# Performance work log

Hardware: AMD Instinct MI355X
Metric: run time of the kernel (lower is better)

## Reference

```python
import jax, jax.numpy as jnp
import numpy as np

N, M, D = 100000, 5000, 2

def setup_inputs() -> dict:
    key = jax.random.key(0)
    k1, k2, k3 = jax.random.split(key, 3)
    euclidean_data = jax.random.normal(k1, (N, D), dtype=jnp.float32)
    maze_points = jax.random.normal(k2, (M, D), dtype=jnp.float32)
    ts_proj = jax.random.uniform(k3, (M,), dtype=jnp.float32)
    return {"euclidean_data": euclidean_data, "maze_points": maze_points, "ts_proj": ts_proj}

def reference(euclidean_data, maze_points, ts_proj):
    # squared distance matrix [N, M], reduced via argmin (1-NN)
    diff = euclidean_data[:, None, :] - maze_points[None, :, :]   # [N, M, D]
    dist2 = jnp.sum(jnp.square(diff), axis=-1)                    # [N, M]
    best = jnp.argmin(dist2, axis=1)                              # [N]
    projected_pos = maze_points[best]                             # [N, D]
    linear_pos = ts_proj[best]                                    # [N]
    return (projected_pos, linear_pos)
```

## Files before the change

### kernel.cpp

```cpp
#include <hip/hip_runtime.h>

#define N_Q  100000
#define N_M  5000
#define CW   4
#define CHK  1264
#define NSUB 79
#define NPAD (CW * CHK)
#define WS_BYTES (NPAD * 2 * 4)

typedef float v2f __attribute__((ext_vector_type(2)));
typedef float v8f __attribute__((ext_vector_type(8)));

__global__ void setup_soa(const float* __restrict__ maze, float* __restrict__ ws) {
    const int i = blockIdx.x * 256 + threadIdx.x;
    if (i >= NPAD) return;
    const int c = i / CHK, k = i - c * CHK;
    float x = 1e30f, y = 1e30f;
    const int g = c * 1250 + k;
    if (k < 1250) { x = -maze[2 * g]; y = -maze[2 * g + 1]; }
    ws[i] = x;
    ws[NPAD + i] = y;
}

#define LDX0(D) asm volatile("s_load_dwordx8 %0, %1, 0x0"    : "=s"(D) : "s"(xb))
#define LDX1(D) asm volatile("s_load_dwordx8 %0, %1, 0x20"   : "=s"(D) : "s"(xb))
#define LDY0(D) asm volatile("s_load_dwordx8 %0, %1, 0x4f00" : "=s"(D) : "s"(xb))
#define LDY1(D) asm volatile("s_load_dwordx8 %0, %1, 0x4f20" : "=s"(D) : "s"(xb))
#define WAIT4(a,b,c,d) asm volatile("s_waitcnt lgkmcnt(0)" : "+s"(a), "+s"(b), "+s"(c), "+s"(d))

#define PSTEP(X8, Y8, J) do {                                                 \
    v2f px_ = __builtin_shufflevector(X8, X8, 2*(J), 2*(J)+1);                \
    v2f py_ = __builtin_shufflevector(Y8, Y8, 2*(J), 2*(J)+1);                \
    v2f dx_, dy_;                                                             \
    asm("v_pk_add_f32 %0, %1, %2" : "=v"(dx_) : "s"(px_), "v"(qxx));          \
    asm("v_pk_add_f32 %0, %1, %2" : "=v"(dy_) : "s"(py_), "v"(qyy));          \
    asm("v_pk_mul_f32 %0, %0, %0" : "+v"(dx_));                               \
    asm("v_pk_mul_f32 %0, %0, %0" : "+v"(dy_));                               \
    asm("v_pk_add_f32 %0, %0, %1" : "+v"(dx_) : "v"(dy_));                    \
    float a_ = dx_.x, b_ = dx_.y;                                             \
    asm("v_min3_f32 %0, %1, %2, %0" : "+v"(bm) : "v"(a_), "v"(b_));           \
} while (0)

#define COMP(X0, X1, Y0, Y1, B) do {                                          \
    PSTEP(X0, Y0, 0); PSTEP(X0, Y0, 1); PSTEP(X0, Y0, 2); PSTEP(X0, Y0, 3);   \
    PSTEP(X1, Y1, 0); PSTEP(X1, Y1, 1); PSTEP(X1, Y1, 2); PSTEP(X1, Y1, 3);   \
    bb = (bm < prev) ? (B) : bb; prev = bm;                                   \
} while (0)

__global__ __launch_bounds__(256) void nn_scan(
    const float* __restrict__ q,
    const float* __restrict__ maze,
    const float* __restrict__ ts,
    const float* __restrict__ ws,
    float* __restrict__ out)
{
    __shared__ float sval[CW][64];
    __shared__ int   sidx[CW][64];

    const int lane = threadIdx.x & 63;
    const int wv   = __builtin_amdgcn_readfirstlane((int)(threadIdx.x >> 6));
    const int qi   = blockIdx.x * 64 + lane;
    const int qc   = qi < N_Q ? qi : N_Q - 1;

    const float2 Q = ((const float2*)q)[qc];
    const v2f qxx = { Q.x, Q.x };
    const v2f qyy = { Q.y, Q.y };

    unsigned long long xb =
        (unsigned long long)(const void*)(ws + (size_t)wv * CHK);

    v8f ax0, ax1, ay0, ay1, bx0, bx1, by0, by1;
    LDX0(ax0); LDX1(ax1); LDY0(ay0); LDY1(ay1); xb += 64;

    float bm = 3.4e38f, prev = 3.4e38f;
    int bb = 0;

    #pragma unroll 1
    for (int k = 0; k < 39; ++k) {
        WAIT4(ax0, ax1, ay0, ay1);
        LDX0(bx0); LDX1(bx1); LDY0(by0); LDY1(by1); xb += 64;
        COMP(ax0, ax1, ay0, ay1, 2 * k);
        WAIT4(bx0, bx1, by0, by1);
        LDX0(ax0); LDX1(ax1); LDY0(ay0); LDY1(ay1); xb += 64;
        COMP(bx0, bx1, by0, by1, 2 * k + 1);
    }
    WAIT4(ax0, ax1, ay0, ay1);
    COMP(ax0, ax1, ay0, ay1, 78);

    int fk = 0x7fffffff;
    {
        const float* xs = ws + (size_t)wv * CHK + (size_t)bb * 16;
        #pragma unroll
        for (int j = 0; j < 16; ++j) {
            const float dx = __fadd_rn(Q.x, xs[j]);
            const float dy = __fadd_rn(Q.y, xs[j + NPAD]);
            const float d2 = __fadd_rn(__fmul_rn(dx, dx), __fmul_rn(dy, dy));
            if (d2 == bm) fk = min(fk, bb * 16 + j);
        }
    }
    const int kloc = fk < 1250 ? fk : 1249;
    sval[wv][lane] = bm;
    sidx[wv][lane] = wv * 1250 + kloc;
    __syncthreads();

    if (wv == 0 && qi < N_Q) {
        float bv = sval[0][lane];
        int   bg = sidx[0][lane];
        #pragma unroll
        for (int c = 1; c < CW; ++c) {
            const float v = sval[c][lane];
            const int   g = sidx[c][lane];
            if (v < bv || (v == bv && g < bg)) { bv = v; bg = g; }
        }
        const float2 bp = ((const float2*)maze)[bg];
        out[2 * qi]       = bp.x;
        out[2 * qi + 1]   = bp.y;
        out[2 * N_Q + qi] = ts[bg];
    }
}

#define FCH   8
#define FLCH  640
#define FNP   (FCH * FLCH)
#define FSUB  16
#define FNSUB (FLCH / FSUB)
#define FFPS  (FSUB / 2)

#define FPK_ADD(d, a, b) asm("v_pk_add_f32 %0, %1, %2" : "=v"(d) : "v"(a), "v"(b))
#define FPK_MUL(d, a, b) asm("v_pk_mul_f32 %0, %1, %2" : "=v"(d) : "v"(a), "v"(b))
#define FMIN3(d, a, b, c) asm("v_min3_f32 %0, %1, %2, %3" : "=v"(d) : "v"(a), "v"(b), "v"(c))

__global__ __launch_bounds__(256) void nn1_fallback(
    const float* __restrict__ q, const float* __restrict__ maze,
    const float* __restrict__ ts, float* __restrict__ out)
{
    __shared__ float4 sm[(FLCH / 2) * FCH];
    const float2* mz = (const float2*)maze;
    for (int i = threadIdx.x; i < FNP; i += 256) {
        const int c = i / FLCH, k = i - c * FLCH;
        float px = 1e30f, py = 1e30f;
        if (i < N_M) { float2 p = mz[i]; px = p.x; py = p.y; }
        ((float2*)sm)[((k >> 1) * FCH + c) * 2 + (k & 1)] = make_float2(-px, -py);
    }
    __syncthreads();
    const int t = threadIdx.x, lane = t & 63, g = lane >> 3, c = lane & 7;
    const int qb = blockIdx.x * 64 + (t >> 6) * 16 + g;
    const int qi0 = qb, qi1 = qb + 8;
    const float2 qa = ((const float2*)q)[qi0 < N_Q ? qi0 : N_Q - 1];
    const float2 qc = ((const float2*)q)[qi1 < N_Q ? qi1 : N_Q - 1];
    const v2f qva = { qa.x, qa.y }, qvb = { qc.x, qc.y };
    const float4* base = &sm[c];
    float run0 = 3.4e38f, run1 = 3.4e38f; int bb0 = 0, bb1 = 0;
    for (int b = 0; b < FNSUB; ++b) {
        float bm0 = 3.4e38f, bm1 = 3.4e38f;
        #pragma unroll
        for (int fi = 0; fi < FFPS; ++fi) {
            const float4 pp = base[(b * FFPS + fi) * FCH];
            const v2f p0 = { pp.x, pp.y }, p1 = { pp.z, pp.w };
            v2f e0, s0, e1, s1, f0, u0, f1, u1;
            FPK_ADD(e0, qva, p0); FPK_MUL(s0, e0, e0);
            FPK_ADD(e1, qva, p1); FPK_MUL(s1, e1, e1);
            FPK_ADD(f0, qvb, p0); FPK_MUL(u0, f0, f0);
            FPK_ADD(f1, qvb, p1); FPK_MUL(u1, f1, f1);
            const float d0a = __fadd_rn(s0.x, s0.y), d1a = __fadd_rn(s1.x, s1.y);
            const float d0b = __fadd_rn(u0.x, u0.y), d1b = __fadd_rn(u1.x, u1.y);
            FMIN3(bm0, d0a, d1a, bm0); FMIN3(bm1, d0b, d1b, bm1);
        }
        if (bm0 < run0) { run0 = bm0; bb0 = b; }
        if (bm1 < run1) { run1 = bm1; bb1 = b; }
    }
    auto rescan = [&](float best, int bbx, v2f qv) -> int {
        int midx = 0x7fffffff;
        #pragma unroll
        for (int fi = 0; fi < FFPS; ++fi) {
            const float4 pp = base[(bbx * FFPS + fi) * FCH];
            const v2f p0 = { pp.x, pp.y }, p1 = { pp.z, pp.w };
            v2f e0, s0, e1, s1;
            FPK_ADD(e0, qv, p0); FPK_MUL(s0, e0, e0);
            FPK_ADD(e1, qv, p1); FPK_MUL(s1, e1, e1);
            const float d0 = __fadd_rn(s0.x, s0.y), d1 = __fadd_rn(s1.x, s1.y);
            const int gi = c * FLCH + bbx * FSUB + fi * 2;
            if (d0 == best && gi < midx) midx = gi;
            if (d1 == best && gi + 1 < midx) midx = gi + 1;
        }
        return midx;
    };
    int mi0 = rescan(run0, bb0, qva), mi1 = rescan(run1, bb1, qvb);
    float v0 = run0, v1 = run1;
    #pragma unroll
    for (int s = 1; s < FCH; s <<= 1) {
        const float o0 = __shfl_xor(v0, s); const int j0 = __shfl_xor(mi0, s);
        if (o0 < v0 || (o0 == v0 && j0 < mi0)) { v0 = o0; mi0 = j0; }
        const float o1 = __shfl_xor(v1, s); const int j1 = __shfl_xor(mi1, s);
        if (o1 < v1 || (o1 == v1 && j1 < mi1)) { v1 = o1; mi1 = j1; }
    }
    if (c == 0) {
        mi0 = mi0 < N_M ? mi0 : N_M - 1; mi1 = mi1 < N_M ? mi1 : N_M - 1;
        if (qi0 < N_Q) { const float2 bp = mz[mi0];
            out[2*qi0] = bp.x; out[2*qi0+1] = bp.y; out[2*N_Q+qi0] = ts[mi0]; }
        if (qi1 < N_Q) { const float2 bp = mz[mi1];
            out[2*qi1] = bp.x; out[2*qi1+1] = bp.y; out[2*N_Q+qi1] = ts[mi1]; }
    }
}

extern "C" void kernel_launch(void* const* d_in, const int* in_sizes, int n_in,
                              void* d_out, int out_size, void* d_ws, size_t ws_size,
                              hipStream_t stream) {
    const float* q    = (const float*)d_in[0];
    const float* maze = (const float*)d_in[1];
    const float* ts   = (const float*)d_in[2];
    float* out = (float*)d_out;

    if (ws_size >= (size_t)WS_BYTES) {
        setup_soa<<<(NPAD + 255) / 256, 256, 0, stream>>>(maze, (float*)d_ws);
        nn_scan<<<(N_Q + 63) / 64, 256, 0, stream>>>(q, maze, ts,
                                                     (const float*)d_ws, out);
    } else {
        nn1_fallback<<<(N_Q + 63) / 64, 256, 0, stream>>>(q, maze, ts, out);
    }
}
```

Measured before the change: 66.04 us.

## Replace brute-force 1-NN scan with uniform grid spatial index plus overflow fallback

Builds a 64x64 uniform grid over the maze points in one block: a bounding-box reduction, a per-cell counting sort, and a prefix scan. Each query then searches rings of cells outward until a distance bound proves its nearest neighbour is found. Queries still unresolved after four rings are appended to a list and brute-forced by wave-per-query kernels. This removes the O(N*M) distance scan, but adds a serial single-block build, divergent per-thread loops and extra launches, and the tie-breaking rule must match argmin exactly.

```diff
diff --git a/kernel.cpp b/kernel.cpp
--- a/kernel.cpp
+++ b/kernel.cpp
@@ -2,11 +2,208 @@
 
 #define N_Q  100000
 #define N_M  5000
+#define G    64
+#define NC   (G * G)
+#define RMAX 4
+#define CS_OFF_B   64
+#define SORT_OFF_B (CS_OFF_B + 16400)
+#define OVF_OFF_B  (SORT_OFF_B + N_M * 16)
+#define WS_NEED    (OVF_OFF_B + N_Q * 4)
+
+__global__ __launch_bounds__(1024) void build_grid(
+    const float* __restrict__ maze, const float* __restrict__ ts,
+    float* __restrict__ ws)
+{
+    __shared__ float red[1024];
+    __shared__ int   part[1024];
+    __shared__ int   cnt[NC];
+    const int t = threadIdx.x;
+    if (t == 0) ((int*)ws)[8] = 0;
+
+    float mnx = 1e30f, mxx = -1e30f, mny = 1e30f, mxy = -1e30f;
+    for (int i = t; i < N_M; i += 1024) {
+        const float x = maze[2 * i], y = maze[2 * i + 1];
+        mnx = fminf(mnx, x); mxx = fmaxf(mxx, x);
+        mny = fminf(mny, y); mxy = fmaxf(mxy, y);
+    }
+    auto reduce = [&](float v, bool domin) -> float {
+        red[t] = v; __syncthreads();
+        for (int s = 512; s > 0; s >>= 1) {
+            if (t < s) {
+                const float o = red[t + s];
+                red[t] = domin ? fminf(red[t], o) : fmaxf(red[t], o);
+            }
+            __syncthreads();
+        }
+        const float r = red[0]; __syncthreads(); return r;
+    };
+    mnx = reduce(mnx, true);  mxx = reduce(mxx, false);
+    mny = reduce(mny, true);  mxy = reduce(mxy, false);
+
+    float cwx = (mxx - mnx) * (1.0f / G) * (1.0f + 1e-5f);
+    float cwy = (mxy - mny) * (1.0f / G) * (1.0f + 1e-5f);
+    if (!(cwx > 0.0f)) cwx = 1.0f;
+    if (!(cwy > 0.0f)) cwy = 1.0f;
+    const float ivx = 1.0f / cwx, ivy = 1.0f / cwy;
+    if (t == 0) {
+        ws[0] = mnx; ws[1] = mny; ws[2] = cwx;
+        ws[3] = cwy; ws[4] = ivx; ws[5] = ivy;
+    }
+
+    for (int i = t; i < NC; i += 1024) cnt[i] = 0;
+    __syncthreads();
+    for (int i = t; i < N_M; i += 1024) {
+        const float x = maze[2 * i], y = maze[2 * i + 1];
+        const int cx = min(G - 1, max(0, (int)((x - mnx) * ivx)));
+        const int cy = min(G - 1, max(0, (int)((y - mny) * ivy)));
+        atomicAdd(&cnt[cy * G + cx], 1);
+    }
+    __syncthreads();
+
+    int* cs = (int*)((char*)ws + CS_OFF_B);
+    const int base = t * 4;
+    int loc[4], sum = 0;
+    #pragma unroll
+    for (int j = 0; j < 4; ++j) { loc[j] = sum; sum += cnt[base + j]; }
+    part[t] = sum; __syncthreads();
+    for (int s = 1; s < 1024; s <<= 1) {
+        const int v = (t >= s) ? part[t - s] : 0;
+        __syncthreads();
+        part[t] += v;
+        __syncthreads();
+    }
+    const int excl = part[t] - sum;
+    #pragma unroll
+    for (int j = 0; j < 4; ++j) cs[base + j] = excl + loc[j];
+    if (t == 0) cs[NC] = N_M;
+    __syncthreads();
+    #pragma unroll
+    for (int j = 0; j < 4; ++j) cnt[base + j] = excl + loc[j];
+    __syncthreads();
+
+    float4* sorted = (float4*)((char*)ws + SORT_OFF_B);
+    for (int i = t; i < N_M; i += 1024) {
+        const float x = maze[2 * i], y = maze[2 * i + 1];
+        const int cx = min(G - 1, max(0, (int)((x - mnx) * ivx)));
+        const int cy = min(G - 1, max(0, (int)((y - mny) * ivy)));
+        const int pos = atomicAdd(&cnt[cy * G + cx], 1);
+        float4 e; e.x = x; e.y = y; e.z = ts[i]; e.w = __int_as_float(i);
+        sorted[pos] = e;
+    }
+}
+
+__global__ __launch_bounds__(256) void grid_query(
+    const float* __restrict__ q, float* __restrict__ ws,
+    float* __restrict__ out)
+{
+    const int qi = blockIdx.x * 256 + threadIdx.x;
+    if (qi >= N_Q) return;
+
+    const float mnx = ws[0], mny = ws[1], cwx = ws[2];
+    const float cwy = ws[3], ivx = ws[4], ivy = ws[5];
+    const int*    cs     = (const int*)((const char*)ws + CS_OFF_B);
+    const float4* sorted = (const float4*)((const char*)ws + SORT_OFF_B);
+
+    const float2 Q = ((const float2*)q)[qi];
+    const float qx = Q.x, qy = Q.y;
+    const int cx = min(G - 1, max(0, (int)((qx - mnx) * ivx)));
+    const int cy = min(G - 1, max(0, (int)((qy - mny) * ivy)));
+
+    float bd2 = 3.4e38f;
+    int bidx = 0x7fffffff, bsp = 0;
+
+    auto scan_pts = [&](int s, int e) {
+        for (int p = s; p < e; ++p) {
+            const float4 c = sorted[p];
+            const float dx = __fsub_rn(qx, c.x);
+            const float dy = __fsub_rn(qy, c.y);
+            const float d2 = __fadd_rn(__fmul_rn(dx, dx), __fmul_rn(dy, dy));
+            const int idx = __float_as_int(c.w);
+            if (d2 < bd2 || (d2 == bd2 && idx < bidx)) { bd2 = d2; bidx = idx; bsp = p; }
+        }
+    };
+    auto scan_row = [&](int rowbase, int xa, int xb) {
+        int prev = cs[rowbase + xa];
+        for (int x = xa; x <= xb; ++x) {
+            const int nxt = cs[rowbase + x + 1];
+            scan_pts(prev, nxt);
+            prev = nxt;
+        }
+    };
+
+    bool resolved = false;
+    for (int r = 0; r <= RMAX; ++r) {
+        const int x0 = max(0, cx - r), x1 = min(G - 1, cx + r);
+        if (r == 0) {
+            scan_row(cy * G, cx, cx);
+        } else {
+            if (cy - r >= 0)     scan_row((cy - r) * G, x0, x1);
+            if (cy + r <= G - 1) scan_row((cy + r) * G, x0, x1);
+            const int yy0 = max(0, cy - r + 1), yy1 = min(G - 1, cy + r - 1);
+            if (cx - r >= 0)     for (int y = yy0; y <= yy1; ++y) { const int c0 = y * G + cx - r; scan_pts(cs[c0], cs[c0 + 1]); }
+            if (cx + r <= G - 1) for (int y = yy0; y <= yy1; ++y) { const int c0 = y * G + cx + r; scan_pts(cs[c0], cs[c0 + 1]); }
+        }
+        const float Xlo = mnx + (float)(cx - r) * cwx;
+        const float Xhi = mnx + (float)(cx + r + 1) * cwx;
+        const float Ylo = mny + (float)(cy - r) * cwy;
+        const float Yhi = mny + (float)(cy + r + 1) * cwy;
+        float lb = fminf(fminf(qx - Xlo, Xhi - qx), fminf(qy - Ylo, Yhi - qy));
+        lb = lb * 0.9999f - 1e-6f;
+        if (lb > 0.0f && lb * lb > bd2) { resolved = true; break; }
+    }
+
+    if (resolved) {
+        const float4 bw = sorted[bsp];
+        out[2 * qi]       = bw.x;
+        out[2 * qi + 1]   = bw.y;
+        out[2 * N_Q + qi] = bw.z;
+    } else {
+        int* ovfc = (int*)ws + 8;
+        const int pos = atomicAdd(ovfc, 1);
+        ((int*)((char*)ws + OVF_OFF_B))[pos] = qi;
+    }
+}
+
+__global__ __launch_bounds__(256) void brute_overflow(
+    const float* __restrict__ q, const float* __restrict__ maze,
+    const float* __restrict__ ts, const float* __restrict__ ws,
+    float* __restrict__ out)
+{
+    const int cnt = ((const int*)ws)[8];
+    const int* ovl = (const int*)((const char*)ws + OVF_OFF_B);
+    const int wave  = (blockIdx.x * 256 + threadIdx.x) >> 6;
+    const int lane  = threadIdx.x & 63;
+    const int nwave = gridDim.x * 4;
+
+    for (int w = wave; w < cnt; w += nwave) {
+        const int qi = ovl[w];
+        const float qx = q[2 * qi], qy = q[2 * qi + 1];
+        float bd2 = 3.4e38f; int bidx = 0x7fffffff;
+        for (int p = lane; p < N_M; p += 64) {
+            const float2 c = ((const float2*)maze)[p];
+            const float dx = __fsub_rn(qx, c.x);
+            const float dy = __fsub_rn(qy, c.y);
+            const float d2 = __fadd_rn(__fmul_rn(dx, dx), __fmul_rn(dy, dy));
+            if (d2 < bd2 || (d2 == bd2 && p < bidx)) { bd2 = d2; bidx = p; }
+        }
+        #pragma unroll
+        for (int s = 1; s < 64; s <<= 1) {
+            const float ob = __shfl_xor(bd2, s);
+            const int   oi = __shfl_xor(bidx, s);
+            if (ob < bd2 || (ob == bd2 && oi < bidx)) { bd2 = ob; bidx = oi; }
+        }
+        if (lane == 0) {
+            out[2 * qi]       = maze[2 * bidx];
+            out[2 * qi + 1]   = maze[2 * bidx + 1];
+            out[2 * N_Q + qi] = ts[bidx];
+        }
+    }
+}
+
 #define CW   4
 #define CHK  1264
-#define NSUB 79
 #define NPAD (CW * CHK)
-#define WS_BYTES (NPAD * 2 * 4)
+#define FB_WS_BYTES (NPAD * 2 * 4)
 
 typedef float v2f __attribute__((ext_vector_type(2)));
 typedef float v8f __attribute__((ext_vector_type(8)));
@@ -48,33 +245,24 @@
 } while (0)
 
 __global__ __launch_bounds__(256) void nn_scan(
-    const float* __restrict__ q,
-    const float* __restrict__ maze,
-    const float* __restrict__ ts,
-    const float* __restrict__ ws,
+    const float* __restrict__ q, const float* __restrict__ maze,
+    const float* __restrict__ ts, const float* __restrict__ ws,
     float* __restrict__ out)
 {
     __shared__ float sval[CW][64];
     __shared__ int   sidx[CW][64];
-
     const int lane = threadIdx.x & 63;
     const int wv   = __builtin_amdgcn_readfirstlane((int)(threadIdx.x >> 6));
     const int qi   = blockIdx.x * 64 + lane;
     const int qc   = qi < N_Q ? qi : N_Q - 1;
-
     const float2 Q = ((const float2*)q)[qc];
     const v2f qxx = { Q.x, Q.x };
     const v2f qyy = { Q.y, Q.y };
-
-    unsigned long long xb =
-        (unsigned long long)(const void*)(ws + (size_t)wv * CHK);
-
+    unsigned long long xb = (unsigned long long)(const void*)(ws + (size_t)wv * CHK);
     v8f ax0, ax1, ay0, ay1, bx0, bx1, by0, by1;
     LDX0(ax0); LDX1(ax1); LDY0(ay0); LDY1(ay1); xb += 64;
-
     float bm = 3.4e38f, prev = 3.4e38f;
     int bb = 0;
-
     #pragma unroll 1
     for (int k = 0; k < 39; ++k) {
         WAIT4(ax0, ax1, ay0, ay1);
@@ -86,7 +274,6 @@
     }
     WAIT4(ax0, ax1, ay0, ay1);
     COMP(ax0, ax1, ay0, ay1, 78);
-
     int fk = 0x7fffffff;
     {
         const float* xs = ws + (size_t)wv * CHK + (size_t)bb * 16;
@@ -102,7 +289,6 @@
     sval[wv][lane] = bm;
     sidx[wv][lane] = wv * 1250 + kloc;
     __syncthreads();
-
     if (wv == 0 && qi < N_Q) {
         float bv = sval[0][lane];
         int   bg = sidx[0][lane];
@@ -119,90 +305,6 @@
     }
 }
 
-#define FCH   8
-#define FLCH  640
-#define FNP   (FCH * FLCH)
-#define FSUB  16
-#define FNSUB (FLCH / FSUB)
-#define FFPS  (FSUB / 2)
-
-#define FPK_ADD(d, a, b) asm("v_pk_add_f32 %0, %1, %2" : "=v"(d) : "v"(a), "v"(b))
-#define FPK_MUL(d, a, b) asm("v_pk_mul_f32 %0, %1, %2" : "=v"(d) : "v"(a), "v"(b))
-#define FMIN3(d, a, b, c) asm("v_min3_f32 %0, %1, %2, %3" : "=v"(d) : "v"(a), "v"(b), "v"(c))
-
-__global__ __launch_bounds__(256) void nn1_fallback(
-    const float* __restrict__ q, const float* __restrict__ maze,
-    const float* __restrict__ ts, float* __restrict__ out)
-{
-    __shared__ float4 sm[(FLCH / 2) * FCH];
-    const float2* mz = (const float2*)maze;
-    for (int i = threadIdx.x; i < FNP; i += 256) {
-        const int c = i / FLCH, k = i - c * FLCH;
-        float px = 1e30f, py = 1e30f;
-        if (i < N_M) { float2 p = mz[i]; px = p.x; py = p.y; }
-        ((float2*)sm)[((k >> 1) * FCH + c) * 2 + (k & 1)] = make_float2(-px, -py);
-    }
-    __syncthreads();
-    const int t = threadIdx.x, lane = t & 63, g = lane >> 3, c = lane & 7;
-    const int qb = blockIdx.x * 64 + (t >> 6) * 16 + g;
-    const int qi0 = qb, qi1 = qb + 8;
-    const float2 qa = ((const float2*)q)[qi0 < N_Q ? qi0 : N_Q - 1];
-    const float2 qc = ((const float2*)q)[qi1 < N_Q ? qi1 : N_Q - 1];
-    const v2f qva = { qa.x, qa.y }, qvb = { qc.x, qc.y };
-    const float4* base = &sm[c];
-    float run0 = 3.4e38f, run1 = 3.4e38f; int bb0 = 0, bb1 = 0;
-    for (int b = 0; b < FNSUB; ++b) {
-        float bm0 = 3.4e38f, bm1 = 3.4e38f;
-        #pragma unroll
-        for (int fi = 0; fi < FFPS; ++fi) {
-            const float4 pp = base[(b * FFPS + fi) * FCH];
-            const v2f p0 = { pp.x, pp.y }, p1 = { pp.z, pp.w };
-            v2f e0, s0, e1, s1, f0, u0, f1, u1;
-            FPK_ADD(e0, qva, p0); FPK_MUL(s0, e0, e0);
-            FPK_ADD(e1, qva, p1); FPK_MUL(s1, e1, e1);
-            FPK_ADD(f0, qvb, p0); FPK_MUL(u0, f0, f0);
-            FPK_ADD(f1, qvb, p1); FPK_MUL(u1, f1, f1);
-            const float d0a = __fadd_rn(s0.x, s0.y), d1a = __fadd_rn(s1.x, s1.y);
-            const float d0b = __fadd_rn(u0.x, u0.y), d1b = __fadd_rn(u1.x, u1.y);
-            FMIN3(bm0, d0a, d1a, bm0); FMIN3(bm1, d0b, d1b, bm1);
-        }
-        if (bm0 < run0) { run0 = bm0; bb0 = b; }
-        if (bm1 < run1) { run1 = bm1; bb1 = b; }
-    }
-    auto rescan = [&](float best, int bbx, v2f qv) -> int {
-        int midx = 0x7fffffff;
-        #pragma unroll
-        for (int fi = 0; fi < FFPS; ++fi) {
-            const float4 pp = base[(bbx * FFPS + fi) * FCH];
-            const v2f p0 = { pp.x, pp.y }, p1 = { pp.z, pp.w };
-            v2f e0, s0, e1, s1;
-            FPK_ADD(e0, qv, p0); FPK_MUL(s0, e0, e0);
-            FPK_ADD(e1, qv, p1); FPK_MUL(s1, e1, e1);
-            const float d0 = __fadd_rn(s0.x, s0.y), d1 = __fadd_rn(s1.x, s1.y);
-            const int gi = c * FLCH + bbx * FSUB + fi * 2;
-            if (d0 == best && gi < midx) midx = gi;
-            if (d1 == best && gi + 1 < midx) midx = gi + 1;
-        }
-        return midx;
-    };
-    int mi0 = rescan(run0, bb0, qva), mi1 = rescan(run1, bb1, qvb);
-    float v0 = run0, v1 = run1;
-    #pragma unroll
-    for (int s = 1; s < FCH; s <<= 1) {
-        const float o0 = __shfl_xor(v0, s); const int j0 = __shfl_xor(mi0, s);
-        if (o0 < v0 || (o0 == v0 && j0 < mi0)) { v0 = o0; mi0 = j0; }
-        const float o1 = __shfl_xor(v1, s); const int j1 = __shfl_xor(mi1, s);
-        if (o1 < v1 || (o1 == v1 && j1 < mi1)) { v1 = o1; mi1 = j1; }
-    }
-    if (c == 0) {
-        mi0 = mi0 < N_M ? mi0 : N_M - 1; mi1 = mi1 < N_M ? mi1 : N_M - 1;
-        if (qi0 < N_Q) { const float2 bp = mz[mi0];
-            out[2*qi0] = bp.x; out[2*qi0+1] = bp.y; out[2*N_Q+qi0] = ts[mi0]; }
-        if (qi1 < N_Q) { const float2 bp = mz[mi1];
-            out[2*qi1] = bp.x; out[2*qi1+1] = bp.y; out[2*N_Q+qi1] = ts[mi1]; }
-    }
-}
-
 extern "C" void kernel_launch(void* const* d_in, const int* in_sizes, int n_in,
                               void* d_out, int out_size, void* d_ws, size_t ws_size,
                               hipStream_t stream) {
@@ -211,11 +313,13 @@
     const float* ts   = (const float*)d_in[2];
     float* out = (float*)d_out;
 
-    if (ws_size >= (size_t)WS_BYTES) {
+    if (ws_size >= (size_t)WS_NEED) {
+        build_grid<<<1, 1024, 0, stream>>>(maze, ts, (float*)d_ws);
+        grid_query<<<(N_Q + 255) / 256, 256, 0, stream>>>(q, (float*)d_ws, out);
+        brute_overflow<<<256, 256, 0, stream>>>(q, maze, ts, (const float*)d_ws, out);
+    } else {
         setup_soa<<<(NPAD + 255) / 256, 256, 0, stream>>>(maze, (float*)d_ws);
         nn_scan<<<(N_Q + 63) / 64, 256, 0, stream>>>(q, maze, ts,
                                                      (const float*)d_ws, out);
-    } else {
-        nn1_fallback<<<(N_Q + 63) / 64, 256, 0, stream>>>(q, maze, ts, out);
-    }
-}
+    }
+}
```

Result: slower. 76.81 us (+16.3%).
